# Kernel tuning notes

Hardware: AMD Instinct MI355X
Metric: run time of the kernel (lower is better)

The kernel has to match this reference:

```python
import jax, jax.numpy as jnp
import numpy as np

EPS = 1e-06


def _cross(a, b):
    return a[..., 0] * b[..., 1] - a[..., 1] * b[..., 0]


def box2corners(box):
    # box: (N,5) = x, y, w, h, alpha -> corners (N,4,2), CCW order
    x, y, w, h, a = (box[:, i] for i in range(5))
    x4 = jnp.array([0.5, -0.5, -0.5, 0.5], box.dtype) * w[:, None]
    y4 = jnp.array([0.5, 0.5, -0.5, -0.5], box.dtype) * h[:, None]
    c, s = jnp.cos(a)[:, None], jnp.sin(a)[:, None]
    return jnp.stack([x4 * c - y4 * s + x[:, None],
                      x4 * s + y4 * c + y[:, None]], axis=-1)


def box_intersection(c1, c2):
    # all 4x4 edge-pair segment intersections; returns (N,16,2) points, (N,16) valid mask
    p1 = c1[:, :, None, :]
    d1 = (jnp.roll(c1, -1, axis=1) - c1)[:, :, None, :]
    p2 = c2[:, None, :, :]
    d2 = (jnp.roll(c2, -1, axis=1) - c2)[:, None, :, :]
    den = _cross(d1, d2)                       # (N,4,4)
    safe = jnp.abs(den) > 1e-12
    den_s = jnp.where(safe, den, 1.0)
    dp = p2 - p1
    t = _cross(dp, d2) / den_s
    u = _cross(dp, d1) / den_s
    mask = safe & (t > 0) & (t < 1) & (u > 0) & (u < 1)
    pts = jnp.where(mask[..., None], p1 + t[..., None] * d1, 0.0)
    n = c1.shape[0]
    return pts.reshape(n, 16, 2), mask.reshape(n, 16)


def box_in_box(c1, c2):
    # which corners of box1 lie inside rectangle box2 (projection test)
    a = c2[:, 0:1]
    ab = c2[:, 1:2] - a
    ad = c2[:, 3:4] - a
    am = c1 - a
    pab = jnp.sum(am * ab, -1) / jnp.maximum(jnp.sum(ab * ab, -1), EPS)
    pad = jnp.sum(am * ad, -1) / jnp.maximum(jnp.sum(ad * ad, -1), EPS)
    tol = 1e-6
    return (pab > -tol) & (pab < 1 + tol) & (pad > -tol) & (pad < 1 + tol)


def intersection_area(c1, c2):
    # candidate vertices: corners of each box inside the other + edge intersections
    ipts, imask = box_intersection(c1, c2)
    v = jnp.concatenate([c1, c2, ipts], axis=1)                      # (N,24,2)
    m = jnp.concatenate([box_in_box(c1, c2), box_in_box(c2, c1), imask], axis=1)
    nv = jnp.sum(m, axis=-1)                                         # num valid
    mf = m.astype(v.dtype)[..., None]
    mean = jnp.sum(v * mf, axis=1) / jnp.maximum(nv, 1)[:, None]
    r = (v - mean[:, None]) * mf                                     # invalid -> 0
    # sort valid vertices CCW by angle around centroid (invalid pushed to end)
    ang = jnp.where(m, jnp.arctan2(r[..., 1], r[..., 0]), 1e6)
    order = jnp.argsort(ang, axis=-1)
    rs = jnp.take_along_axis(r, order[..., None], axis=1)            # (N,24,2)
    # shoelace over consecutive pairs; invalid entries are zero so contribute 0
    area2 = jnp.sum(_cross(rs[:, :-1], rs[:, 1:]), axis=1)
    # closure term: last valid vertex -> first vertex
    idx = jnp.broadcast_to(jnp.maximum(nv - 1, 0)[:, None, None], (v.shape[0], 1, 2))
    r_last = jnp.take_along_axis(rs, idx, axis=1)[:, 0]
    area2 = area2 + _cross(r_last, rs[:, 0])
    return 0.5 * jnp.abs(area2)


def setup_inputs() -> dict:
    key = jax.random.key(0)
    k1, k2, k3, k4, k5 = jax.random.split(key, 5)
    N = 1_000_000
    cxy = jax.random.uniform(k1, (N, 2), jnp.float32) * 1024.0
    wh = jax.random.uniform(k2, (N, 2), jnp.float32) * 60.0 + 4.0
    ang = jax.random.uniform(k3, (N, 1), jnp.float32) * jnp.pi
    pred = jnp.concatenate([cxy, wh, ang], axis=1)
    noise = jax.random.normal(k4, (N, 5), jnp.float32) * jnp.array([3.0, 3.0, 2.0, 2.0, 0.1], jnp.float32)
    target = pred + noise
    target = target.at[:, 2:4].set(jnp.clip(target[:, 2:4], 1.0))
    weight = jax.random.uniform(k5, (N,), jnp.float32)
    return {"pred": pred, "target": target, "weight": weight}


def reference(pred, target, weight):
    loss_weight = 1.0
    c1 = box2corners(pred)
    c2 = box2corners(target)
    inter = intersection_area(c1, c2)
    a1 = pred[:, 2] * pred[:, 3]
    a2 = target[:, 2] * target[:, 3]
    ious = jnp.clip(inter / (a1 + a2 - inter), EPS)
    center_distance = (pred[:, 0] - target[:, 0]) ** 2 + (pred[:, 1] - target[:, 1]) ** 2
    aspect = (4.0 / jnp.pi ** 2) * (jnp.arctan(target[:, 2] / (target[:, 3] + EPS))
                                    - jnp.arctan(pred[:, 2] / (pred[:, 3] + EPS))) ** 2
    v = aspect / (1.0 - ious + aspect)
    alpha = v / (1.0 - ious + v)
    loss = 1.0 - ious + center_distance / (pred[:, 2] ** 2 + pred[:, 3] ** 2 + EPS) + alpha * v
    # weighted_loss with weight, reduction='mean', avg_factor=None
    return loss_weight * jnp.mean(loss * weight)
```

## Files before the change

kernel.cpp:

```cpp
#include <hip/hip_runtime.h>
#include <math.h>

#define EPSF 1e-6f

__device__ __forceinline__ float block_reduce_sum(float v) {
    #pragma unroll
    for (int off = 32; off > 0; off >>= 1)
        v += __shfl_down(v, off, 64);
    __shared__ float smem[4];
    int lane = threadIdx.x & 63;
    int wid  = threadIdx.x >> 6;
    if (lane == 0) smem[wid] = v;
    __syncthreads();
    float s = 0.0f;
    if (threadIdx.x == 0) {
        #pragma unroll
        for (int w = 0; w < 4; w++) s += smem[w];
    }
    return s;
}

__global__ void __launch_bounds__(256)
ciou_loss_kernel(const float* __restrict__ pred,
                 const float* __restrict__ target,
                 const float* __restrict__ weight,
                 float* __restrict__ partial,
                 int N)
{
    __shared__ float2 poly[2][8][256];

    int tid = threadIdx.x;
    int idx = blockIdx.x * 256 + tid;
    float contrib = 0.0f;
    if (idx < N) {
        const float* p = pred   + (size_t)idx * 5;
        const float* t = target + (size_t)idx * 5;
        float px = p[0], py = p[1], pw = p[2], ph = p[3], pa = p[4];
        float tx = t[0], ty = t[1], tw = t[2], th = t[3], ta = t[4];

        const float sgx[4] = { 0.5f, -0.5f, -0.5f,  0.5f };
        const float sgy[4] = { 0.5f,  0.5f, -0.5f, -0.5f };
        float c2x[4], c2y[4];
        float ca, sa, cb, sb;
        __sincosf(pa, &sa, &ca);
        __sincosf(ta, &sb, &cb);
        #pragma unroll
        for (int i = 0; i < 4; i++) {
            float x4 = sgx[i] * pw, y4 = sgy[i] * ph;
            poly[0][i][tid] = make_float2(x4 * ca - y4 * sa + px,
                                          x4 * sa + y4 * ca + py);
        }
        #pragma unroll
        for (int i = 0; i < 4; i++) {
            float x4 = sgx[i] * tw, y4 = sgy[i] * th;
            c2x[i] = x4 * cb - y4 * sb + tx;
            c2y[i] = x4 * sb + y4 * cb + ty;
        }

        int cur = 0, n = 4;
        #pragma unroll
        for (int e = 0; e < 4; e++) {
            float ax = c2x[e], ay = c2y[e];
            float ex = c2x[(e + 1) & 3] - ax;
            float ey = c2y[(e + 1) & 3] - ay;
            int m = 0;
            if (n > 0) {
                float2 first = poly[cur][0][tid];
                float2 C = first;
                float dc = ex * (C.y - ay) - ey * (C.x - ax);
                for (int k = 0; k < n; k++) {
                    float2 D;
                    if (k + 1 == n) D = first;
                    else            D = poly[cur][k + 1][tid];
                    float dd = ex * (D.y - ay) - ey * (D.x - ax);
                    bool cin = (dc >= 0.0f), din = (dd >= 0.0f);
                    if (cin && m < 8) { poly[cur ^ 1][m][tid] = C; m++; }
                    if (cin != din && m < 8) {
                        float tt = dc / (dc - dd);
                        poly[cur ^ 1][m][tid] =
                            make_float2(C.x + tt * (D.x - C.x), C.y + tt * (D.y - C.y));
                        m++;
                    }
                    C = D; dc = dd;
                }
            }
            cur ^= 1;
            n = m;
        }

        float area2 = 0.0f;
        if (n >= 3) {
            float2 first = poly[cur][0][tid];
            float2 prev = first;
            for (int k = 1; k < n; k++) {
                float2 v = poly[cur][k][tid];
                area2 += prev.x * v.y - prev.y * v.x;
                prev = v;
            }
            area2 += prev.x * first.y - prev.y * first.x;
        }
        float inter = 0.5f * fabsf(area2);

        float a1 = pw * ph, a2 = tw * th;
        float iou = inter / (a1 + a2 - inter);
        iou = fmaxf(iou, EPSF);
        float dx0 = px - tx, dy0 = py - ty;
        float cd = dx0 * dx0 + dy0 * dy0;
        float da = atanf(tw / (th + EPSF)) - atanf(pw / (ph + EPSF));
        const float c4pi2 = 4.0f / (3.14159265358979323846f * 3.14159265358979323846f);
        float aspect = c4pi2 * da * da;
        float vterm = aspect / (1.0f - iou + aspect);
        float alpha = vterm / (1.0f - iou + vterm);
        float loss = 1.0f - iou + cd / (pw * pw + ph * ph + EPSF) + alpha * vterm;
        contrib = loss * weight[idx];
    }

    float s = block_reduce_sum(contrib);
    if (threadIdx.x == 0) partial[blockIdx.x] = s;
}

__global__ void __launch_bounds__(256)
reduce_final_kernel(const float* __restrict__ partial, int nparts, float invN,
                    float* __restrict__ out)
{
    float s = 0.0f;
    for (int i = threadIdx.x; i < nparts; i += 256) s += partial[i];
    s = block_reduce_sum(s);
    if (threadIdx.x == 0) out[0] = s * invN;
}

extern "C" void kernel_launch(void* const* d_in, const int* in_sizes, int n_in,
                              void* d_out, int out_size, void* d_ws, size_t ws_size,
                              hipStream_t stream) {
    const float* pred   = (const float*)d_in[0];
    const float* target = (const float*)d_in[1];
    const float* weight = (const float*)d_in[2];
    int N = in_sizes[2];
    float* partial = (float*)d_ws;

    int blocks = (N + 255) / 256;
    ciou_loss_kernel<<<blocks, 256, 0, stream>>>(pred, target, weight, partial, N);
    reduce_final_kernel<<<1, 256, 0, stream>>>(partial, blocks, 1.0f / (float)N,
                                               (float*)d_out);
}
```

Before: 110.6 us.

## Replace shared-memory polygon clipping with branchless edge-clipped Green's theorem area

Swaps the Sutherland-Hodgman clipping loop, which kept the polygon in LDS, for a register-only formulation. Each edge of each box is clipped against the other box's half-planes with a Cyrus-Beck parametric clip, and the clipped segments' cross products are summed to get twice the intersection area. Coordinates are re-centred on the midpoint of the two box centres to reduce cancellation error. This removes LDS traffic, data-dependent loops and divergence, at the cost of a fixed, larger amount of arithmetic and higher register pressure.

```diff
diff --git a/kernel.cpp b/kernel.cpp
--- a/kernel.cpp
+++ b/kernel.cpp
@@ -27,8 +27,6 @@
                  float* __restrict__ partial,
                  int N)
 {
-    __shared__ float2 poly[2][8][256];
-
     int tid = threadIdx.x;
     int idx = blockIdx.x * 256 + tid;
     float contrib = 0.0f;
@@ -38,67 +36,93 @@
         float px = p[0], py = p[1], pw = p[2], ph = p[3], pa = p[4];
         float tx = t[0], ty = t[1], tw = t[2], th = t[3], ta = t[4];
 
+        float cx0 = 0.5f * (px + tx), cy0 = 0.5f * (py + ty);
+
         const float sgx[4] = { 0.5f, -0.5f, -0.5f,  0.5f };
         const float sgy[4] = { 0.5f,  0.5f, -0.5f, -0.5f };
-        float c2x[4], c2y[4];
+        float Pxv[4], Pyv[4], Qxv[4], Qyv[4];
         float ca, sa, cb, sb;
         __sincosf(pa, &sa, &ca);
         __sincosf(ta, &sb, &cb);
         #pragma unroll
         for (int i = 0; i < 4; i++) {
             float x4 = sgx[i] * pw, y4 = sgy[i] * ph;
-            poly[0][i][tid] = make_float2(x4 * ca - y4 * sa + px,
-                                          x4 * sa + y4 * ca + py);
+            Pxv[i] = x4 * ca - y4 * sa + (px - cx0);
+            Pyv[i] = x4 * sa + y4 * ca + (py - cy0);
+            float u4 = sgx[i] * tw, v4 = sgy[i] * th;
+            Qxv[i] = u4 * cb - v4 * sb + (tx - cx0);
+            Qyv[i] = u4 * sb + v4 * cb + (ty - cy0);
         }
+
+        float Pex[4], Pey[4], Qex[4], Qey[4];
         #pragma unroll
         for (int i = 0; i < 4; i++) {
-            float x4 = sgx[i] * tw, y4 = sgy[i] * th;
-            c2x[i] = x4 * cb - y4 * sb + tx;
-            c2y[i] = x4 * sb + y4 * cb + ty;
+            Pex[i] = Pxv[(i + 1) & 3] - Pxv[i];
+            Pey[i] = Pyv[(i + 1) & 3] - Pyv[i];
+            Qex[i] = Qxv[(i + 1) & 3] - Qxv[i];
+            Qey[i] = Qyv[(i + 1) & 3] - Qyv[i];
         }
 
-        int cur = 0, n = 4;
+        float dPQ[4][4], dQP[4][4];
         #pragma unroll
-        for (int e = 0; e < 4; e++) {
-            float ax = c2x[e], ay = c2y[e];
-            float ex = c2x[(e + 1) & 3] - ax;
-            float ey = c2y[(e + 1) & 3] - ay;
-            int m = 0;
-            if (n > 0) {
-                float2 first = poly[cur][0][tid];
-                float2 C = first;
-                float dc = ex * (C.y - ay) - ey * (C.x - ax);
-                for (int k = 0; k < n; k++) {
-                    float2 D;
-                    if (k + 1 == n) D = first;
-                    else            D = poly[cur][k + 1][tid];
-                    float dd = ex * (D.y - ay) - ey * (D.x - ax);
-                    bool cin = (dc >= 0.0f), din = (dd >= 0.0f);
-                    if (cin && m < 8) { poly[cur ^ 1][m][tid] = C; m++; }
-                    if (cin != din && m < 8) {
-                        float tt = dc / (dc - dd);
-                        poly[cur ^ 1][m][tid] =
-                            make_float2(C.x + tt * (D.x - C.x), C.y + tt * (D.y - C.y));
-                        m++;
-                    }
-                    C = D; dc = dd;
-                }
+        for (int i = 0; i < 4; i++) {
+            #pragma unroll
+            for (int j = 0; j < 4; j++) {
+                dPQ[i][j] = Qex[j] * (Pyv[i] - Qyv[j]) - Qey[j] * (Pxv[i] - Qxv[j]);
+                dQP[i][j] = Pex[j] * (Qyv[i] - Pyv[j]) - Pey[j] * (Qxv[i] - Pxv[j]);
             }
-            cur ^= 1;
-            n = m;
         }
 
         float area2 = 0.0f;
-        if (n >= 3) {
-            float2 first = poly[cur][0][tid];
-            float2 prev = first;
-            for (int k = 1; k < n; k++) {
-                float2 v = poly[cur][k][tid];
-                area2 += prev.x * v.y - prev.y * v.x;
-                prev = v;
+
+        #pragma unroll
+        for (int i = 0; i < 4; i++) {
+            int ip = (i + 1) & 3;
+            float Cx = Pxv[i], Cy = Pyv[i];
+            float ex = Pex[i], ey = Pey[i];
+            float t0 = 0.0f, t1 = 1.0f;
+            #pragma unroll
+            for (int j = 0; j < 4; j++) {
+                float dc = dPQ[i][j], dd = dPQ[ip][j];
+                float denom = dc - dd;
+                bool  par   = fabsf(denom) < 1e-12f;
+                float ds    = par ? 1.0f : denom;
+                float tt    = dc * __builtin_amdgcn_rcpf(ds);
+                bool  enter = denom < 0.0f;
+                t0 = (!par &&  enter) ? fmaxf(t0, tt) : t0;
+                t1 = (!par && !enter) ? fminf(t1, tt) : t1;
+                t1 = (par && dc < 0.0f) ? -1.0f : t1;
             }
-            area2 += prev.x * first.y - prev.y * first.x;
+            float t1c = fmaxf(t1, t0);
+            float Ax = Cx + t0  * ex, Ay = Cy + t0  * ey;
+            float Bx = Cx + t1c * ex, By = Cy + t1c * ey;
+            area2 += Ax * By - Ay * Bx;
         }
+
+        #pragma unroll
+        for (int i = 0; i < 4; i++) {
+            int ip = (i + 1) & 3;
+            float Cx = Qxv[i], Cy = Qyv[i];
+            float ex = Qex[i], ey = Qey[i];
+            float t0 = 0.0f, t1 = 1.0f;
+            #pragma unroll
+            for (int j = 0; j < 4; j++) {
+                float dc = dQP[i][j], dd = dQP[ip][j];
+                float denom = dc - dd;
+                bool  par   = fabsf(denom) < 1e-12f;
+                float ds    = par ? 1.0f : denom;
+                float tt    = dc * __builtin_amdgcn_rcpf(ds);
+                bool  enter = denom < 0.0f;
+                t0 = (!par &&  enter) ? fmaxf(t0, tt) : t0;
+                t1 = (!par && !enter) ? fminf(t1, tt) : t1;
+                t1 = (par && dc < 0.0f) ? -1.0f : t1;
+            }
+            float t1c = fmaxf(t1, t0);
+            float Ax = Cx + t0  * ex, Ay = Cy + t0  * ey;
+            float Bx = Cx + t1c * ex, By = Cy + t1c * ey;
+            area2 += Ax * By - Ay * Bx;
+        }
+
         float inter = 0.5f * fabsf(area2);
 
         float a1 = pw * ph, a2 = tw * th;
```

Measured after the change: 102.8 us. 1.08x faster.
